# Kernel optimization log

Hardware: AMD Instinct MI355X
Metric: run time of the kernel (lower is better)

Reference implementation:

```python
import jax, jax.numpy as jnp
import numpy as np

DOUT_P = 0.1
MEAN_FACTOR = 10.0
STD_FACTOR = 5.0


def setup_inputs() -> dict:
    key = jax.random.key(0)
    k1, k2, k3, k4 = jax.random.split(key, 4)
    B, S, D, G = 32, 4096, 512, 128
    x = jax.random.normal(k1, (B, S, D), dtype=jnp.float32)
    critic_mask = jax.random.randint(k2, (B, S), 0, 2).astype(bool)
    # torch nn.Linear weight layout: [out_features, in_features]
    W = jax.random.normal(k3, (G, D), dtype=jnp.float32) * (1.0 / np.sqrt(D))
    b = jax.random.normal(k4, (G,), dtype=jnp.float32) * 0.01
    return {"x": x, "critic_mask": critic_mask, "W": W, "b": b}


def _forward(x, critic_mask, W, b):
    # --- dropout (deterministic key for reproducibility) ---
    kd, kn = jax.random.split(jax.random.key(42))
    keep = jax.random.bernoulli(kd, 1.0 - DOUT_P, x.shape)
    x = jnp.where(keep, x / (1.0 - DOUT_P), jnp.zeros((), x.dtype))
    # --- linear: [B,S,D] @ [G,D]^T + b -> [B,S,G] ---
    h = jnp.einsum('bsd,gd->bsg', x, W) + b
    # --- exploration noise (std/mean detached, per torch.std unbiased) ---
    std = jax.lax.stop_gradient(jnp.std(h, ddof=1) / STD_FACTOR)
    mean = jax.lax.stop_gradient(jnp.mean(h) / MEAN_FACTOR)
    G = h.shape[-1]
    noise = mean + std * jax.random.normal(kn, (G,), dtype=h.dtype) - 0.5 * mean
    h = h + noise
    # --- expand_goals: segment forward-fill as cummax + gather ---
    # position t (t>=1) starts a new segment iff critic_mask[b, t-1]; position 0 always starts.
    B, S, _ = h.shape
    idx = jnp.arange(S, dtype=jnp.int32)
    starts = jnp.concatenate([jnp.ones((B, 1), bool), critic_mask[:, :-1]], axis=1)  # [B,S]
    last_start = jax.lax.cummax(jnp.where(starts, idx[None, :], 0), axis=1)  # [B,S]
    out = jnp.take_along_axis(h, last_start[:, :, None], axis=1)  # [B,S,G]
    return out


def reference(x, critic_mask, W, b):
    return _forward(x, critic_mask, W, b)
```

## Files before the change

kernel.cpp:

```cpp
#include <hip/hip_runtime.h>
#include <stdint.h>
#include <math.h>

#define B_ 32
#define S_ 4096
#define D_ 512
#define G_ 128
#define MROWS (B_ * S_)
#define NTOT (16777216.0)

#define PARTITIONABLE 1

typedef __attribute__((ext_vector_type(8))) short bf16x8;
typedef __attribute__((ext_vector_type(4))) float f32x4;

__host__ __device__ __forceinline__ uint32_t rotl32(uint32_t x, int r) {
  return (x << r) | (x >> (32 - r));
}

__host__ __device__ __forceinline__ void threefry2x32(
    uint32_t k0, uint32_t k1, uint32_t x0, uint32_t x1,
    uint32_t& o0, uint32_t& o1) {
  const uint32_t ks2 = k0 ^ k1 ^ 0x1BD11BDAu;
  uint32_t v0 = x0 + k0;
  uint32_t v1 = x1 + k1;
#define TF_RND(r) { v0 += v1; v1 = rotl32(v1, (r)); v1 ^= v0; }
  TF_RND(13) TF_RND(15) TF_RND(26) TF_RND(6)
  v0 += k1;  v1 += ks2 + 1u;
  TF_RND(17) TF_RND(29) TF_RND(16) TF_RND(24)
  v0 += ks2; v1 += k0 + 2u;
  TF_RND(13) TF_RND(15) TF_RND(26) TF_RND(6)
  v0 += k0;  v1 += k1 + 3u;
  TF_RND(17) TF_RND(29) TF_RND(16) TF_RND(24)
  v0 += k1;  v1 += ks2 + 4u;
  TF_RND(13) TF_RND(15) TF_RND(26) TF_RND(6)
  v0 += ks2; v1 += k0 + 5u;
#undef TF_RND
  o0 = v0; o1 = v1;
}

__device__ __forceinline__ float bits_to_u01(uint32_t bits) {
  return __uint_as_float((bits >> 9) | 0x3f800000u) - 1.0f;
}

__device__ __forceinline__ float drop_scale(uint32_t kd0, uint32_t kd1,
                                            uint32_t j, float xv) {
  uint32_t o0, o1;
  threefry2x32(kd0, kd1, 0u, j, o0, o1);
  uint32_t bits = o0 ^ o1;
  float u = bits_to_u01(bits);
  return (u < 0.9f) ? (xv / 0.9f) : 0.0f;
}

__device__ __forceinline__ void split_bf16(float v, ushort& hh, ushort& ll) {
  uint32_t u = __float_as_uint(v);
  uint32_t rh = (u + 0x7FFFu + ((u >> 16) & 1u)) >> 16;
  hh = (ushort)rh;
  float hf = __uint_as_float(rh << 16);
  float lf = v - hf;
  uint32_t ul = __float_as_uint(lf);
  ll = (ushort)((ul + 0x7FFFu + ((ul >> 16) & 1u)) >> 16);
}

__device__ __forceinline__ bool mask_at(const void* m, int mode, long long i) {
  if (mode == 0) return ((const int*)m)[i] != 0;
  if (mode == 1) return ((const unsigned char*)m)[i] != 0;
  return ((const float*)m)[i] != 0.0f;
}

__device__ __forceinline__ int probe_mode(const void* mask) {
  const uint32_t* wm = (const uint32_t*)mask;
  bool all01 = true, allf = true;
  for (int i = 0; i < 64; ++i) {
    uint32_t w = wm[i];
    if (w > 1u) all01 = false;
    if (w != 0u && w != 0x3f800000u) allf = false;
  }
  return all01 ? 0 : (allf ? 2 : 1);
}

__global__ __launch_bounds__(256, 2) void k_matmul(
    const float* __restrict__ x, const float* __restrict__ Wm,
    const float* __restrict__ bias, float* __restrict__ h,
    double* __restrict__ sums, uint32_t kd0, uint32_t kd1)
{
  __shared__ ushort AsH[128][40];
  __shared__ ushort AsL[128][40];
  __shared__ ushort BsH[128][40];
  __shared__ ushort BsL[128][40];
  __shared__ double red[8];

  const int tid = threadIdx.x;
  const long long row0 = (long long)blockIdx.x * 128;

  f32x4 acc[4][4];
#pragma unroll
  for (int m = 0; m < 4; ++m)
#pragma unroll
    for (int n = 0; n < 4; ++n) acc[m][n] = (f32x4)0.0f;

  const int arow = tid >> 1;
  const int ak0  = (tid & 1) << 4;
  const float* xrow = x + (row0 + arow) * D_ + ak0;
  const float* wrow = Wm + arow * D_ + ak0;
  const uint32_t jrow = (uint32_t)((row0 + arow) * D_) + (uint32_t)ak0;

  const int lane = tid & 63;
  const int wid  = tid >> 6;
  const int rbw  = (wid >> 1) * 64;
  const int cbw  = (wid & 1) * 64;
  const int lr   = lane & 15;
  const int lk   = (lane >> 4) * 8;

  float4 ax0, ax1, ax2, ax3, wx0, wx1, wx2, wx3;
#define LOADT(kc) { \
    const float4* xp = (const float4*)(xrow + (kc)); \
    const float4* wp = (const float4*)(wrow + (kc)); \
    ax0 = xp[0]; ax1 = xp[1]; ax2 = xp[2]; ax3 = xp[3]; \
    wx0 = wp[0]; wx1 = wp[1]; wx2 = wp[2]; wx3 = wp[3]; }

#define PROCA(xv, i4, kc) { \
    uint32_t jb = jrow + (uint32_t)(kc) + (uint32_t)((i4) * 4); \
    float v0 = drop_scale(kd0, kd1, jb + 0u, (xv).x); \
    float v1 = drop_scale(kd0, kd1, jb + 1u, (xv).y); \
    float v2 = drop_scale(kd0, kd1, jb + 2u, (xv).z); \
    float v3 = drop_scale(kd0, kd1, jb + 3u, (xv).w); \
    ushort h0,l0,h1,l1,h2,l2,h3,l3; \
    split_bf16(v0,h0,l0); split_bf16(v1,h1,l1); \
    split_bf16(v2,h2,l2); split_bf16(v3,h3,l3); \
    *(ushort4*)&AsH[arow][ak0 + (i4)*4] = make_ushort4(h0,h1,h2,h3); \
    *(ushort4*)&AsL[arow][ak0 + (i4)*4] = make_ushort4(l0,l1,l2,l3); }

#define PROCW(wv, i4) { \
    ushort h0,l0,h1,l1,h2,l2,h3,l3; \
    split_bf16((wv).x,h0,l0); split_bf16((wv).y,h1,l1); \
    split_bf16((wv).z,h2,l2); split_bf16((wv).w,h3,l3); \
    *(ushort4*)&BsH[arow][ak0 + (i4)*4] = make_ushort4(h0,h1,h2,h3); \
    *(ushort4*)&BsL[arow][ak0 + (i4)*4] = make_ushort4(l0,l1,l2,l3); }

  LOADT(0);
  for (int kc = 0; kc < D_; kc += 32) {
    PROCA(ax0, 0, kc) PROCA(ax1, 1, kc) PROCA(ax2, 2, kc) PROCA(ax3, 3, kc)
    PROCW(wx0, 0) PROCW(wx1, 1) PROCW(wx2, 2) PROCW(wx3, 3)
    __syncthreads();
    if (kc + 32 < D_) LOADT(kc + 32);

    bf16x8 ah[4], al[4], bh[4], bl[4];
#pragma unroll
    for (int m = 0; m < 4; ++m) {
      ah[m] = *(const bf16x8*)&AsH[rbw + m * 16 + lr][lk];
      al[m] = *(const bf16x8*)&AsL[rbw + m * 16 + lr][lk];
    }
#pragma unroll
    for (int n = 0; n < 4; ++n) {
      bh[n] = *(const bf16x8*)&BsH[cbw + n * 16 + lr][lk];
      bl[n] = *(const bf16x8*)&BsL[cbw + n * 16 + lr][lk];
    }
#pragma unroll
    for (int m = 0; m < 4; ++m)
#pragma unroll
      for (int n = 0; n < 4; ++n) {
        acc[m][n] = __builtin_amdgcn_mfma_f32_16x16x32_bf16(ah[m], bh[n], acc[m][n], 0, 0, 0);
        acc[m][n] = __builtin_amdgcn_mfma_f32_16x16x32_bf16(ah[m], bl[n], acc[m][n], 0, 0, 0);
        acc[m][n] = __builtin_amdgcn_mfma_f32_16x16x32_bf16(al[m], bh[n], acc[m][n], 0, 0, 0);
      }
    __syncthreads();
  }
#undef LOADT
#undef PROCA
#undef PROCW

  double s1 = 0.0, s2 = 0.0;
  const int orow_q = (lane >> 4) * 4;
  float bn[4];
#pragma unroll
  for (int n = 0; n < 4; ++n) bn[n] = bias[cbw + n * 16 + lr];
#pragma unroll
  for (int m = 0; m < 4; ++m) {
#pragma unroll
    for (int n = 0; n < 4; ++n) {
#pragma unroll
      for (int r = 0; r < 4; ++r) {
        const long long grow = row0 + rbw + m * 16 + orow_q + r;
        float v = acc[m][n][r] + bn[n];
        h[grow * G_ + cbw + n * 16 + lr] = v;
        s1 += (double)v;
        s2 += (double)v * (double)v;
      }
    }
  }
#pragma unroll
  for (int off = 32; off > 0; off >>= 1) {
    s1 += __shfl_down(s1, off);
    s2 += __shfl_down(s2, off);
  }
  if (lane == 0) { red[wid * 2] = s1; red[wid * 2 + 1] = s2; }
  __syncthreads();
  if (tid == 0) {
    atomicAdd(&sums[0], red[0] + red[2] + red[4] + red[6]);
    atomicAdd(&sums[1], red[1] + red[3] + red[5] + red[7]);
  }
}

__global__ void k_noise(const void* __restrict__ mask,
                        const double* __restrict__ sums,
                        float* __restrict__ noise, int* __restrict__ mode_p,
                        uint32_t kn0, uint32_t kn1)
{
  const int g = threadIdx.x;
  const double S1 = sums[0], S2 = sums[1];
  const float meanf = (float)(S1 / NTOT);
  const double var = (S2 - S1 * S1 / NTOT) / (NTOT - 1.0);
  const float stdf = (float)sqrt(var);
  const float mean_s = meanf / 10.0f;
  const float std_s  = stdf / 5.0f;

  uint32_t o0, o1;
  threefry2x32(kn0, kn1, 0u, (uint32_t)g, o0, o1);
  uint32_t bits = o0 ^ o1;
  float u = bits_to_u01(bits);
  float v = u * 2.0f + (-0.99999994f);
  v = fmaxf(v, -0.99999994f);
  float wv = -log1pf(-v * v);
  float p;
  if (wv < 5.0f) {
    wv -= 2.5f;
    p = 2.81022636e-08f;
    p = fmaf(p, wv, 3.43273939e-07f);
    p = fmaf(p, wv, -3.5233877e-06f);
    p = fmaf(p, wv, -4.39150654e-06f);
    p = fmaf(p, wv, 0.00021858087f);
    p = fmaf(p, wv, -0.00125372503f);
    p = fmaf(p, wv, -0.00417768164f);
    p = fmaf(p, wv, 0.246640727f);
    p = fmaf(p, wv, 1.50140941f);
  } else {
    wv = sqrtf(wv) - 3.0f;
    p = -0.000200214257f;
    p = fmaf(p, wv, 0.000100950558f);
    p = fmaf(p, wv, 0.00134934322f);
    p = fmaf(p, wv, -0.00367342844f);
    p = fmaf(p, wv, 0.00573950773f);
    p = fmaf(p, wv, -0.0076224613f);
    p = fmaf(p, wv, 0.00943887047f);
    p = fmaf(p, wv, 1.00167406f);
    p = fmaf(p, wv, 2.83297682f);
  }
  const float nrm = 1.41421354f * (p * v);
  noise[g] = mean_s + std_s * nrm - 0.5f * mean_s;

  if (g == 0) *mode_p = probe_mode(mask);
}

__global__ __launch_bounds__(256) void k_scan(const void* __restrict__ mask,
                                              int* __restrict__ ls)
{
  __shared__ int tm[256];
  __shared__ int smode;
  const int b = blockIdx.x, tid = threadIdx.x;
  if (tid == 0) smode = probe_mode(mask);
  __syncthreads();
  const int mode = smode;
  const long long mb = (long long)b * S_;
  const int base = tid * 16;
  int run = 0;
#pragma unroll
  for (int i = 0; i < 16; ++i) {
    int t = base + i;
    if (t == 0 || mask_at(mask, mode, mb + t - 1)) run = t;
  }
  int cur = run;
  tm[tid] = cur;
  __syncthreads();
  for (int off = 1; off < 256; off <<= 1) {
    int o = (tid >= off) ? tm[tid - off] : 0;
    __syncthreads();
    cur = max(cur, o);
    tm[tid] = cur;
    __syncthreads();
  }
  int pref = (tid > 0) ? tm[tid - 1] : 0;
  run = pref;
#pragma unroll
  for (int i = 0; i < 16; ++i) {
    int t = base + i;
    if (t == 0 || mask_at(mask, mode, mb + t - 1)) run = t;
    ls[mb + t] = run;
  }
}

__global__ void k_addnoise_ls(float* __restrict__ h,
                              const int* __restrict__ ls,
                              const float* __restrict__ noise)
{
  const long long idx4 = (long long)blockIdx.x * blockDim.x + threadIdx.x;
  const long long row = idx4 >> 5;
  const int t = (int)(row & (S_ - 1));
  if (ls[row] != t) return;
  const int c4 = (int)(idx4 & 31);
  const float4 nv = ((const float4*)noise)[c4];
  float4 v = ((float4*)h)[idx4];
  v.x += nv.x; v.y += nv.y; v.z += nv.z; v.w += nv.w;
  ((float4*)h)[idx4] = v;
}

__global__ void k_gather_ls(float* __restrict__ h, const int* __restrict__ ls)
{
  const long long row = (long long)blockIdx.x * 8 + (threadIdx.x >> 5);
  const int c4 = threadIdx.x & 31;
  const int t = (int)(row & (S_ - 1));
  const int s = ls[row];
  if (s == t) return;
  const long long b = row >> 12;
  const float4 v = ((const float4*)h)[((b << 12) + s) * 32 + c4];
  ((float4*)h)[row * 32 + c4] = v;
}

__global__ void k_addnoise(float* __restrict__ h, const void* __restrict__ mask,
                           const float* __restrict__ noise,
                           const int* __restrict__ mode_p)
{
  const int mode = *mode_p;
  const long long idx4 = (long long)blockIdx.x * blockDim.x + threadIdx.x;
  const long long row = idx4 >> 5;
  const int t = (int)(row & (S_ - 1));
  const long long b = row >> 12;
  const bool start = (t == 0) || mask_at(mask, mode, b * S_ + t - 1);
  if (!start) return;
  const int c4 = (int)(idx4 & 31);
  const float4 nv = ((const float4*)noise)[c4];
  float4 v = ((float4*)h)[idx4];
  v.x += nv.x; v.y += nv.y; v.z += nv.z; v.w += nv.w;
  ((float4*)h)[idx4] = v;
}

__global__ void k_fill(float* __restrict__ h, const void* __restrict__ mask,
                       const int* __restrict__ mode_p)
{
  const int mode = *mode_p;
  const long long row = (long long)blockIdx.x * 8 + (threadIdx.x >> 5);
  const int lane4 = threadIdx.x & 31;
  const int t = (int)(row & (S_ - 1));
  const long long b = row >> 12;
  const long long mbase = b * S_;
  int s = t;
  while (s > 0 && !mask_at(mask, mode, mbase + s - 1)) --s;
  if (s == t) return;
  const float4 v = ((const float4*)h)[(mbase + s) * 32 + lane4];
  ((float4*)h)[row * 32 + lane4] = v;
}

extern "C" void kernel_launch(void* const* d_in, const int* in_sizes, int n_in,
                              void* d_out, int out_size, void* d_ws, size_t ws_size,
                              hipStream_t stream)
{
  (void)in_sizes; (void)n_in; (void)out_size;
  const float* x    = (const float*)d_in[0];
  const void*  mask = d_in[1];
  const float* Wm   = (const float*)d_in[2];
  const float* bias = (const float*)d_in[3];
  float* h = (float*)d_out;

  double* sums  = (double*)d_ws;
  int*    modep = (int*)((char*)d_ws + 16);
  float*  noise = (float*)((char*)d_ws + 32);
  int*    ls    = (int*)((char*)d_ws + 1024);
  const bool bigws = ws_size >= (size_t)(1024 + MROWS * 4);

  uint32_t kd0, kd1, kn0, kn1;
  threefry2x32(0u, 42u, 0u, 0u, kd0, kd1);
  threefry2x32(0u, 42u, 0u, 1u, kn0, kn1);

  hipMemsetAsync(d_ws, 0, 16, stream);
  if (bigws)
    hipLaunchKernelGGL(k_scan, dim3(B_), dim3(256), 0, stream, mask, ls);
  hipLaunchKernelGGL(k_matmul, dim3(MROWS / 128), dim3(256), 0, stream,
                     x, Wm, bias, h, sums, kd0, kd1);
  hipLaunchKernelGGL(k_noise, dim3(1), dim3(128), 0, stream,
                     mask, sums, noise, modep, kn0, kn1);
  if (bigws) {
    hipLaunchKernelGGL(k_addnoise_ls, dim3((MROWS * 32) / 256), dim3(256), 0, stream,
                       h, ls, noise);
    hipLaunchKernelGGL(k_gather_ls, dim3(MROWS / 8), dim3(256), 0, stream, h, ls);
  } else {
    hipLaunchKernelGGL(k_addnoise, dim3((MROWS * 32) / 256), dim3(256), 0, stream,
                       h, mask, noise, modep);
    hipLaunchKernelGGL(k_fill, dim3(MROWS / 8), dim3(256), 0, stream, h, mask, modep);
  }
}
```

Measured before the change: 521.1 us.

## Replace global scan pipeline with per-block warp scan fill and ballot mode probe

Removes the separate k_scan kernel and the global last-start index buffer. Each fill block now computes its own forward-fill sources for 64 rows with a wavefront shuffle scan, walking back through earlier chunks to find a carry when needed. The mask-type probe becomes a ballot, the dropout test uses an integer compare with a reciprocal multiply, the bf16 high split truncates instead of rounding, and matmul launch bounds rise to 3 blocks per CU. This saves a kernel launch and the index traffic. The risks are register spills at the higher occupancy target and long backward searches when segments are long.

Result: faster. 483.4 us (-7.2%).

```diff
diff --git a/kernel.cpp b/kernel.cpp
--- a/kernel.cpp
+++ b/kernel.cpp
@@ -8,8 +8,6 @@
 #define G_ 128
 #define MROWS (B_ * S_)
 #define NTOT (16777216.0)
-
-#define PARTITIONABLE 1
 
 typedef __attribute__((ext_vector_type(8))) short bf16x8;
 typedef __attribute__((ext_vector_type(4))) float f32x4;
@@ -47,17 +45,14 @@
                                             uint32_t j, float xv) {
   uint32_t o0, o1;
   threefry2x32(kd0, kd1, 0u, j, o0, o1);
-  uint32_t bits = o0 ^ o1;
-  float u = bits_to_u01(bits);
-  return (u < 0.9f) ? (xv / 0.9f) : 0.0f;
+  uint32_t m = (o0 ^ o1) >> 9;
+  return (m < 7549747u) ? xv * 1.11111116f : 0.0f;
 }
 
 __device__ __forceinline__ void split_bf16(float v, ushort& hh, ushort& ll) {
   uint32_t u = __float_as_uint(v);
-  uint32_t rh = (u + 0x7FFFu + ((u >> 16) & 1u)) >> 16;
-  hh = (ushort)rh;
-  float hf = __uint_as_float(rh << 16);
-  float lf = v - hf;
+  hh = (ushort)(u >> 16);
+  float lf = v - __uint_as_float(u & 0xFFFF0000u);
   uint32_t ul = __float_as_uint(lf);
   ll = (ushort)((ul + 0x7FFFu + ((ul >> 16) & 1u)) >> 16);
 }
@@ -68,18 +63,7 @@
   return ((const float*)m)[i] != 0.0f;
 }
 
-__device__ __forceinline__ int probe_mode(const void* mask) {
-  const uint32_t* wm = (const uint32_t*)mask;
-  bool all01 = true, allf = true;
-  for (int i = 0; i < 64; ++i) {
-    uint32_t w = wm[i];
-    if (w > 1u) all01 = false;
-    if (w != 0u && w != 0x3f800000u) allf = false;
-  }
-  return all01 ? 0 : (allf ? 2 : 1);
-}
-
-__global__ __launch_bounds__(256, 2) void k_matmul(
+__global__ __launch_bounds__(256, 3) void k_matmul(
     const float* __restrict__ x, const float* __restrict__ Wm,
     const float* __restrict__ bias, float* __restrict__ h,
     double* __restrict__ sums, uint32_t kd0, uint32_t kd1)
@@ -249,71 +233,12 @@
   const float nrm = 1.41421354f * (p * v);
   noise[g] = mean_s + std_s * nrm - 0.5f * mean_s;
 
-  if (g == 0) *mode_p = probe_mode(mask);
-}
-
-__global__ __launch_bounds__(256) void k_scan(const void* __restrict__ mask,
-                                              int* __restrict__ ls)
-{
-  __shared__ int tm[256];
-  __shared__ int smode;
-  const int b = blockIdx.x, tid = threadIdx.x;
-  if (tid == 0) smode = probe_mode(mask);
-  __syncthreads();
-  const int mode = smode;
-  const long long mb = (long long)b * S_;
-  const int base = tid * 16;
-  int run = 0;
-#pragma unroll
-  for (int i = 0; i < 16; ++i) {
-    int t = base + i;
-    if (t == 0 || mask_at(mask, mode, mb + t - 1)) run = t;
-  }
-  int cur = run;
-  tm[tid] = cur;
-  __syncthreads();
-  for (int off = 1; off < 256; off <<= 1) {
-    int o = (tid >= off) ? tm[tid - off] : 0;
-    __syncthreads();
-    cur = max(cur, o);
-    tm[tid] = cur;
-    __syncthreads();
-  }
-  int pref = (tid > 0) ? tm[tid - 1] : 0;
-  run = pref;
-#pragma unroll
-  for (int i = 0; i < 16; ++i) {
-    int t = base + i;
-    if (t == 0 || mask_at(mask, mode, mb + t - 1)) run = t;
-    ls[mb + t] = run;
-  }
-}
-
-__global__ void k_addnoise_ls(float* __restrict__ h,
-                              const int* __restrict__ ls,
-                              const float* __restrict__ noise)
-{
-  const long long idx4 = (long long)blockIdx.x * blockDim.x + threadIdx.x;
-  const long long row = idx4 >> 5;
-  const int t = (int)(row & (S_ - 1));
-  if (ls[row] != t) return;
-  const int c4 = (int)(idx4 & 31);
-  const float4 nv = ((const float4*)noise)[c4];
-  float4 v = ((float4*)h)[idx4];
-  v.x += nv.x; v.y += nv.y; v.z += nv.z; v.w += nv.w;
-  ((float4*)h)[idx4] = v;
-}
-
-__global__ void k_gather_ls(float* __restrict__ h, const int* __restrict__ ls)
-{
-  const long long row = (long long)blockIdx.x * 8 + (threadIdx.x >> 5);
-  const int c4 = threadIdx.x & 31;
-  const int t = (int)(row & (S_ - 1));
-  const int s = ls[row];
-  if (s == t) return;
-  const long long b = row >> 12;
-  const float4 v = ((const float4*)h)[((b << 12) + s) * 32 + c4];
-  ((float4*)h)[row * 32 + c4] = v;
+  if (g < 64) {
+    uint32_t w = ((const uint32_t*)mask)[g];
+    unsigned long long b01 = __ballot(w > 1u);
+    unsigned long long bfl = __ballot(w != 0u && w != 0x3f800000u);
+    if (g == 0) *mode_p = (b01 == 0ull) ? 0 : ((bfl == 0ull) ? 2 : 1);
+  }
 }
 
 __global__ void k_addnoise(float* __restrict__ h, const void* __restrict__ mask,
@@ -334,27 +259,61 @@
   ((float4*)h)[idx4] = v;
 }
 
-__global__ void k_fill(float* __restrict__ h, const void* __restrict__ mask,
-                       const int* __restrict__ mode_p)
-{
+__global__ __launch_bounds__(256) void k_fill2(float* __restrict__ h,
+                                               const void* __restrict__ mask,
+                                               const int* __restrict__ mode_p)
+{
+  __shared__ int ls_s[64];
   const int mode = *mode_p;
-  const long long row = (long long)blockIdx.x * 8 + (threadIdx.x >> 5);
-  const int lane4 = threadIdx.x & 31;
-  const int t = (int)(row & (S_ - 1));
-  const long long b = row >> 12;
-  const long long mbase = b * S_;
-  int s = t;
-  while (s > 0 && !mask_at(mask, mode, mbase + s - 1)) --s;
-  if (s == t) return;
-  const float4 v = ((const float4*)h)[(mbase + s) * 32 + lane4];
-  ((float4*)h)[row * 32 + lane4] = v;
+  const int bidx = blockIdx.x;
+  const int b = bidx >> 6;
+  const int t0 = (bidx & 63) << 6;
+  const long long mb = (long long)b * S_;
+  const int tid = threadIdx.x;
+
+  if (tid < 64) {
+    const int lane = tid;
+    const int t = t0 + lane;
+    const bool flag = (t == 0) || mask_at(mask, mode, mb + t - 1);
+    int val = flag ? t : -1;
+#pragma unroll
+    for (int off = 1; off < 64; off <<= 1) {
+      int v2 = __shfl_up(val, off);
+      if (lane >= off) val = max(val, v2);
+    }
+    unsigned long long need = __ballot(val == -1);
+    if (need) {
+      int carry = 0;
+      for (int w = 1;; ++w) {
+        const int tp = t0 - (w << 6) + lane;
+        const bool fp = (tp == 0) || (tp > 0 && mask_at(mask, mode, mb + tp - 1));
+        unsigned long long bal = __ballot(fp);
+        if (bal) { carry = t0 - (w << 6) + (63 - __clzll(bal)); break; }
+      }
+      if (val == -1) val = carry;
+    }
+    ls_s[lane] = val;
+  }
+  __syncthreads();
+
+  float4* h4 = (float4*)h;
+  const int c4 = tid & 31;
+  const int rbase = tid >> 5;
+#pragma unroll
+  for (int it = 0; it < 8; ++it) {
+    const int rl = rbase + it * 8;
+    const int s = ls_s[rl];
+    const int t = t0 + rl;
+    if (s != t)
+      h4[(mb + t) * 32 + c4] = h4[(mb + s) * 32 + c4];
+  }
 }
 
 extern "C" void kernel_launch(void* const* d_in, const int* in_sizes, int n_in,
                               void* d_out, int out_size, void* d_ws, size_t ws_size,
                               hipStream_t stream)
 {
-  (void)in_sizes; (void)n_in; (void)out_size;
+  (void)in_sizes; (void)n_in; (void)out_size; (void)ws_size;
   const float* x    = (const float*)d_in[0];
   const void*  mask = d_in[1];
   const float* Wm   = (const float*)d_in[2];
@@ -364,27 +323,18 @@
   double* sums  = (double*)d_ws;
   int*    modep = (int*)((char*)d_ws + 16);
   float*  noise = (float*)((char*)d_ws + 32);
-  int*    ls    = (int*)((char*)d_ws + 1024);
-  const bool bigws = ws_size >= (size_t)(1024 + MROWS * 4);
 
   uint32_t kd0, kd1, kn0, kn1;
   threefry2x32(0u, 42u, 0u, 0u, kd0, kd1);
   threefry2x32(0u, 42u, 0u, 1u, kn0, kn1);
 
   hipMemsetAsync(d_ws, 0, 16, stream);
-  if (bigws)
-    hipLaunchKernelGGL(k_scan, dim3(B_), dim3(256), 0, stream, mask, ls);
   hipLaunchKernelGGL(k_matmul, dim3(MROWS / 128), dim3(256), 0, stream,
                      x, Wm, bias, h, sums, kd0, kd1);
   hipLaunchKernelGGL(k_noise, dim3(1), dim3(128), 0, stream,
                      mask, sums, noise, modep, kn0, kn1);
-  if (bigws) {
-    hipLaunchKernelGGL(k_addnoise_ls, dim3((MROWS * 32) / 256), dim3(256), 0, stream,
-                       h, ls, noise);
-    hipLaunchKernelGGL(k_gather_ls, dim3(MROWS / 8), dim3(256), 0, stream, h, ls);
-  } else {
-    hipLaunchKernelGGL(k_addnoise, dim3((MROWS * 32) / 256), dim3(256), 0, stream,
-                       h, mask, noise, modep);
-    hipLaunchKernelGGL(k_fill, dim3(MROWS / 8), dim3(256), 0, stream, h, mask, modep);
-  }
-}
+  hipLaunchKernelGGL(k_addnoise, dim3((MROWS * 32) / 256), dim3(256), 0, stream,
+                     h, mask, noise, modep);
+  hipLaunchKernelGGL(k_fill2, dim3(B_ * 64), dim3(256), 0, stream,
+                     h, mask, modep);
+}
```
